# Performance work log

Measured on AMD Instinct MI355X. Metric: run time of the kernel, lower is better.

The kernel has to match this reference:

```python
import jax, jax.numpy as jnp
from jax import lax
import numpy as np

D, E, N, L = 192, 384, 16, 2
P_SZ, IMG, C_IN, K = 16, 224, 3, 3
NP = (IMG // P_SZ) ** 2          # 196 patches
M = NP + 1                        # +cls token
BATCH = 8


def setup_inputs() -> dict:
    key = jax.random.key(0)
    ks = iter(jax.random.split(key, 40))
    nrm = lambda shape, s=0.02: jax.random.normal(next(ks), shape, jnp.float32) * s
    inp = {
        "img": jax.random.normal(next(ks), (BATCH, C_IN, IMG, IMG), jnp.float32),
        "patch_w": nrm((C_IN * P_SZ * P_SZ, D)),
        "patch_b": jnp.zeros((D,), jnp.float32),
        "cls": jnp.zeros((1, 1, D), jnp.float32),
        "pos": nrm((1, M, D)),
        # per-layer stacked params (leading dim L)
        "ln_g": jnp.ones((L, D), jnp.float32), "ln_b": jnp.zeros((L, D), jnp.float32),
        "Wx": nrm((L, D, E)), "bx": jnp.zeros((L, E), jnp.float32),
        "Wz": nrm((L, D, E)), "bz": jnp.zeros((L, E), jnp.float32),
        "cwf": nrm((L, E, 1, K), 0.1), "cbf": jnp.zeros((L, E), jnp.float32),
        "cwb": nrm((L, E, 1, K), 0.1), "cbb": jnp.zeros((L, E), jnp.float32),
        "WBf": nrm((L, E, E * N)), "bBf": jnp.zeros((L, E * N), jnp.float32),
        "WCf": nrm((L, E, E * N)), "bCf": jnp.zeros((L, E * N), jnp.float32),
        "WDf": jnp.zeros((L, E, E), jnp.float32), "bDf": jnp.zeros((L, E), jnp.float32),
        "Af": nrm((L, E, N), 0.01), "dbf": jnp.zeros((L, E), jnp.float32),
        "WBb": nrm((L, E, E * N)), "bBb": jnp.zeros((L, E * N), jnp.float32),
        "WCb": nrm((L, E, E * N)), "bCb": jnp.zeros((L, E * N), jnp.float32),
        "WDb": jnp.zeros((L, E, E), jnp.float32), "bDb": jnp.zeros((L, E), jnp.float32),
        "Ab": nrm((L, E, N), 0.01), "dbb": jnp.zeros((L, E), jnp.float32),
        "Wout": nrm((L, E, D)), "bout": jnp.zeros((L, D), jnp.float32),
        "ng": jnp.ones((D,), jnp.float32), "nb": jnp.zeros((D,), jnp.float32),
    }
    return inp


def layernorm(x, g, b, eps=1e-5):
    mu = x.mean(-1, keepdims=True)
    var = ((x - mu) ** 2).mean(-1, keepdims=True)
    return (x - mu) * lax.rsqrt(var + eps) * g + b


def dwconv(x, w, b):
    # x: (B, M, E), w: (E, 1, K) depthwise, 'same' padding
    xc = jnp.transpose(x, (0, 2, 1))  # (B, E, M)
    pad = (w.shape[-1] - 1) // 2
    y = lax.conv_general_dilated(xc, w, (1,), [(pad, pad)],
                                 dimension_numbers=("NCH", "OIH", "NCH"),
                                 feature_group_count=w.shape[0])
    return jnp.transpose(y, (0, 2, 1)) + b


def ssm_recurrence(A, Bm, Cm, x):
    # A,Bm,Cm: (B,M,E,N); x: (B,M,E). Log-space prefix-product scan.
    eps = 1e-6
    signA = jnp.sign(A)
    absA = jnp.clip(jnp.abs(A), eps)
    logP = jnp.cumsum(jnp.log(absA), axis=1)
    P = jnp.cumprod(signA, axis=1) * jnp.exp(logP)
    invP = 1.0 / (P + eps)
    S = jnp.cumsum(invP * Bm * x[..., None], axis=1)
    h = P * S
    return (h * Cm).sum(-1)  # (B, M, E)


def vim_block(x, p, i):
    Bsz, Mseq, _ = x.shape
    xn = layernorm(x, p["ln_g"][i], p["ln_b"][i])
    xp = xn @ p["Wx"][i] + p["bx"][i]
    z = xn @ p["Wz"][i] + p["bz"][i]
    xf = jax.nn.silu(dwconv(xp, p["cwf"][i], p["cbf"][i]))
    xb = jax.nn.silu(dwconv(xp[:, ::-1], p["cwb"][i], p["cbb"][i])[:, ::-1])

    def branch(xs, WB, bB, WC, bC, WD, bD, Apar, db):
        Bm = (xs @ WB + bB).reshape(Bsz, Mseq, E, N)
        Cm = (xs @ WC + bC).reshape(Bsz, Mseq, E, N)
        Delta = jax.nn.softplus(xs @ WD + bD + db)          # (B,M,E)
        Afull = Delta[..., None] * Apar[None, None]          # (B,M,E,N)
        Bfull = Delta[..., None] * Bm
        return ssm_recurrence(Afull, Bfull, Cm, xs)

    y_f = branch(xf, p["WBf"][i], p["bBf"][i], p["WCf"][i], p["bCf"][i],
                 p["WDf"][i], p["bDf"][i], p["Af"][i], p["dbf"][i])
    y_b = branch(xb, p["WBb"][i], p["bBb"][i], p["WCb"][i], p["bCb"][i],
                 p["WDb"][i], p["bDb"][i], p["Ab"][i], p["dbb"][i])
    g = jax.nn.silu(z)
    y = (y_f + y_b) * g
    return y @ p["Wout"][i] + p["bout"][i] + x


def reference(img, patch_w, patch_b, cls, pos, ln_g, ln_b, Wx, bx, Wz, bz,
              cwf, cbf, cwb, cbb, WBf, bBf, WCf, bCf, WDf, bDf, Af, dbf,
              WBb, bBb, WCb, bCb, WDb, bDb, Ab, dbb, Wout, bout, ng, nb):
    Bsz = img.shape[0]
    hn = IMG // P_SZ
    # patchify (equivalent to Conv2d kernel=stride=patch): (B,3,H,W)->(B,NP,3*p*p)
    patches = img.reshape(Bsz, C_IN, hn, P_SZ, hn, P_SZ)
    patches = patches.transpose(0, 2, 4, 1, 3, 5).reshape(Bsz, NP, C_IN * P_SZ * P_SZ)
    x = patches @ patch_w + patch_b                           # (B,NP,D)
    x = jnp.concatenate([jnp.broadcast_to(cls, (Bsz, 1, D)), x], axis=1)
    x = x + pos
    p = dict(ln_g=ln_g, ln_b=ln_b, Wx=Wx, bx=bx, Wz=Wz, bz=bz, cwf=cwf, cbf=cbf,
             cwb=cwb, cbb=cbb, WBf=WBf, bBf=bBf, WCf=WCf, bCf=bCf, WDf=WDf,
             bDf=bDf, Af=Af, dbf=dbf, WBb=WBb, bBb=bBb, WCb=WCb, bCb=bCb,
             WDb=WDb, bDb=bDb, Ab=Ab, dbb=dbb, Wout=Wout, bout=bout)
    for i in range(L):
        x = vim_block(x, p, i)
    return layernorm(x, ng, nb)  # (B, M, D)
```

## Files before the change

### kernel.cpp

```cpp
#include <hip/hip_runtime.h>
#include <hip/hip_bf16.h>
#include <math.h>

#define BATCH   8
#define C_IN    3
#define IMG_SZ  224
#define P_SZ    16
#define NPATCH  196
#define MSEQ    197
#define DDIM    192
#define EDIM    384
#define NSTATE  16
#define ENDIM   (EDIM*NSTATE)
#define LLAYERS 2
#define ROWS    (BATCH*MSEQ)
#define PROWS   (BATCH*NPATCH)
#define PATCH_K (C_IN*P_SZ*P_SZ)
#define AP_ROWS 1664
#define MFRAGS  52
#define NFRAGS  192
#define KBLKS   24
#define FRAG    512

typedef unsigned short u16;
typedef __attribute__((ext_vector_type(8))) short bf16x8;
typedef __attribute__((ext_vector_type(16))) float f32x16;

__device__ __forceinline__ float silu_f(float x) { return x / (1.f + expf(-x)); }

__device__ __forceinline__ u16 f2bf(float f) {
    unsigned u = __float_as_uint(f);
    unsigned r = (u + 0x7FFFu + ((u >> 16) & 1u)) >> 16;
    return (u16)r;
}
__device__ __forceinline__ float bf2f(u16 h) {
    return __uint_as_float(((unsigned)h) << 16);
}

__global__ __launch_bounds__(256) void patchify_k(const float* __restrict__ img,
                                                  float* __restrict__ out) {
    int idx = blockIdx.x * 256 + threadIdx.x;
    if (idx >= PROWS * PATCH_K) return;
    int r = idx / PATCH_K, col = idx - r * PATCH_K;
    int b = r / NPATCH, p = r - b * NPATCH;
    int ph = p / 14, pw = p - ph * 14;
    int c = col >> 8, rem = col & 255, py = rem >> 4, px = rem & 15;
    out[idx] = img[((b * C_IN + c) * IMG_SZ + ph * P_SZ + py) * IMG_SZ + pw * P_SZ + px];
}

__global__ __launch_bounds__(256) void assemble_k(const float* __restrict__ xemb,
                                                  const float* __restrict__ cls,
                                                  const float* __restrict__ pos,
                                                  float* __restrict__ x) {
    int idx = blockIdx.x * 256 + threadIdx.x;
    if (idx >= ROWS * DDIM) return;
    int d = idx % DDIM;
    int bm = idx / DDIM;
    int m = bm % MSEQ, b = bm / MSEQ;
    float v;
    if (m == 0) v = cls[d];
    else        v = xemb[((b * NPATCH) + (m - 1)) * DDIM + d];
    x[idx] = v + pos[m * DDIM + d];
}

__global__ __launch_bounds__(256) void layernorm_k(const float* __restrict__ x,
                                                   const float* __restrict__ g,
                                                   const float* __restrict__ b,
                                                   float* __restrict__ o, int nrows) {
    int wave = threadIdx.x >> 6;
    int lane = threadIdx.x & 63;
    int row = blockIdx.x * 4 + wave;
    if (row >= nrows) return;
    const float* xr = x + (long)row * DDIM;
    float v0 = xr[lane], v1 = xr[lane + 64], v2 = xr[lane + 128];
    float s = v0 + v1 + v2;
    #pragma unroll
    for (int off = 1; off < 64; off <<= 1) s += __shfl_xor(s, off);
    float mu = s * (1.f / 192.f);
    float d0 = v0 - mu, d1 = v1 - mu, d2 = v2 - mu;
    float q = d0 * d0 + d1 * d1 + d2 * d2;
    #pragma unroll
    for (int off = 1; off < 64; off <<= 1) q += __shfl_xor(q, off);
    float inv = rsqrtf(q * (1.f / 192.f) + 1e-5f);
    float* orow = o + (long)row * DDIM;
    orow[lane]       = d0 * inv * g[lane]       + b[lane];
    orow[lane + 64]  = d1 * inv * g[lane + 64]  + b[lane + 64];
    orow[lane + 128] = d2 * inv * g[lane + 128] + b[lane + 128];
}

__global__ __launch_bounds__(256) void convA_k(const float* __restrict__ xf,
                                               const float* __restrict__ xb,
                                               u16* __restrict__ Af3,
                                               u16* __restrict__ Ab3) {
    int idx = blockIdx.x * 256 + threadIdx.x;
    if (idx >= MFRAGS * KBLKS * 64) return;
    int lane = idx & 63;
    int kb = (idx >> 6) % KBLKS;
    int mf = idx / (64 * KBLKS);
    int row = mf * 32 + (lane & 31);
    int k = kb * 16 + (lane >> 5) * 8;
    long fo = ((long)mf * KBLKS + kb) * FRAG + (long)lane * 8;
    const long plane = (long)MFRAGS * KBLKS * FRAG;
    #pragma unroll
    for (int s = 0; s < 2; ++s) {
        const float* src = s ? xb : xf;
        u16* out = s ? Ab3 : Af3;
        uint4 hq = {0,0,0,0}, mq = {0,0,0,0}, lq = {0,0,0,0};
        if (row < ROWS) {
            u16* hp = (u16*)&hq; u16* mp = (u16*)&mq; u16* lp = (u16*)&lq;
            const float* xr = src + (long)row * EDIM + k;
            #pragma unroll
            for (int j = 0; j < 8; ++j) {
                float x = xr[j];
                u16 hb = f2bf(x);        float fh = bf2f(hb);
                float r1 = x - fh;
                u16 mb = f2bf(r1);       float fm = bf2f(mb);
                u16 lb = f2bf(r1 - fm);
                hp[j] = hb; mp[j] = mb; lp[j] = lb;
            }
        }
        *(uint4*)&out[fo] = hq;
        *(uint4*)&out[plane + fo] = mq;
        *(uint4*)&out[2 * plane + fo] = lq;
    }
}

__global__ __launch_bounds__(256) void convWt_k(const float* __restrict__ W0,
                                                const float* __restrict__ W1,
                                                const float* __restrict__ W2,
                                                const float* __restrict__ W3,
                                                u16* __restrict__ Wt) {
    int z = blockIdx.z;
    const float* W = (z == 0) ? W0 : (z == 1) ? W1 : (z == 2) ? W2 : W3;
    const long plane = (long)NFRAGS * KBLKS * FRAG;
    u16* out = Wt + (long)z * 3L * plane;
    __shared__ float tile[64][65];
    int n0 = blockIdx.x * 64, k0 = blockIdx.y * 64;
    int t = threadIdx.x;
    #pragma unroll
    for (int i = 0; i < 16; ++i) {
        int id = t + 256 * i;
        int kk = id >> 6, nn = id & 63;
        tile[kk][nn] = W[(long)(k0 + kk) * ENDIM + n0 + nn];
    }
    __syncthreads();
    #pragma unroll
    for (int i = 0; i < 2; ++i) {
        int id = t + 256 * i;
        int nn = id >> 3, ch = id & 7;
        int n = n0 + nn;
        int kc = k0 + ch * 8;
        int nf = n >> 5, l31 = n & 31;
        int kb = kc >> 4, l5 = (kc >> 3) & 1;
        uint4 hq, mq, lq;
        u16* hp = (u16*)&hq; u16* mp = (u16*)&mq; u16* lp = (u16*)&lq;
        #pragma unroll
        for (int j = 0; j < 8; ++j) {
            float x = tile[ch * 8 + j][nn];
            u16 hb = f2bf(x);        float fh = bf2f(hb);
            float r1 = x - fh;
            u16 mb = f2bf(r1);       float fm = bf2f(mb);
            u16 lb = f2bf(r1 - fm);
            hp[j] = hb; mp[j] = mb; lp[j] = lb;
        }
        long fo = ((long)nf * KBLKS + kb) * FRAG + (long)(l5 * 32 + l31) * 8;
        *(uint4*)&out[fo] = hq;
        *(uint4*)&out[plane + fo] = mq;
        *(uint4*)&out[2 * plane + fo] = lq;
    }
}

__global__ __launch_bounds__(256) void gemm_mfma(
        const u16* __restrict__ A3,
        const u16* __restrict__ Wt0, const float* __restrict__ b0, float* __restrict__ C0,
        const u16* __restrict__ Wt1, const float* __restrict__ b1, float* __restrict__ C1) {
    const u16* Wt     = blockIdx.z ? Wt1 : Wt0;
    const float* bias = blockIdx.z ? b1 : b0;
    float* C          = blockIdx.z ? C1 : C0;
    int t = threadIdx.x;
    int lane = t & 63, wv = t >> 6;
    int wr = wv >> 1, wc = wv & 1;
    int l31 = lane & 31, l5 = lane >> 5;
    int mf0 = blockIdx.y * 4 + wr * 2;
    int nf0 = blockIdx.x * 4 + wc * 2;
    const u16* Ab = A3 + (long)lane * 8;
    const u16* Wb = Wt + (long)lane * 8;
    f32x16 acc[2][2] = {};

    for (int kb = 0; kb < KBLKS; ++kb) {
        bf16x8 af[2][3], wf[2][3];
        #pragma unroll
        for (int r = 0; r < 2; ++r)
            #pragma unroll
            for (int p = 0; p < 3; ++p)
                af[r][p] = *(const bf16x8*)(Ab + (((long)p * MFRAGS + mf0 + r) * KBLKS + kb) * FRAG);
        #pragma unroll
        for (int c = 0; c < 2; ++c)
            #pragma unroll
            for (int p = 0; p < 3; ++p)
                wf[c][p] = *(const bf16x8*)(Wb + (((long)p * NFRAGS + nf0 + c) * KBLKS + kb) * FRAG);
        #pragma unroll
        for (int r = 0; r < 2; ++r)
            #pragma unroll
            for (int c = 0; c < 2; ++c) {
                f32x16 d = acc[r][c];
                d = __builtin_amdgcn_mfma_f32_32x32x16_bf16(af[r][0], wf[c][0], d, 0, 0, 0);
                d = __builtin_amdgcn_mfma_f32_32x32x16_bf16(af[r][0], wf[c][1], d, 0, 0, 0);
                d = __builtin_amdgcn_mfma_f32_32x32x16_bf16(af[r][1], wf[c][0], d, 0, 0, 0);
                d = __builtin_amdgcn_mfma_f32_32x32x16_bf16(af[r][0], wf[c][2], d, 0, 0, 0);
                d = __builtin_amdgcn_mfma_f32_32x32x16_bf16(af[r][2], wf[c][0], d, 0, 0, 0);
                d = __builtin_amdgcn_mfma_f32_32x32x16_bf16(af[r][1], wf[c][1], d, 0, 0, 0);
                acc[r][c] = d;
            }
    }
    int rowBase = blockIdx.y * 128;
    long colBase = (long)blockIdx.x * 128;
    #pragma unroll
    for (int r = 0; r < 2; ++r) {
        int rb = rowBase + wr * 64 + r * 32 + 4 * l5;
        #pragma unroll
        for (int c = 0; c < 2; ++c) {
            long cb = colBase + wc * 64 + c * 32 + l31;
            float bv = bias[cb];
            #pragma unroll
            for (int i = 0; i < 16; ++i) {
                int rr = rb + (i & 3) + 8 * (i >> 2);
                if (rr < ROWS) C[(long)rr * ENDIM + cb] = acc[r][c][i] + bv;
            }
        }
    }
}

#define SBK 16
template<bool SP, bool HASB2, bool HASRES>
__global__ __launch_bounds__(64) void gemm_s(const float* __restrict__ A0,
                                             const float* __restrict__ W0,
                                             const float* __restrict__ b10,
                                             const float* __restrict__ b20,
                                             const float* __restrict__ r0,
                                             float* __restrict__ C0,
                                             const float* __restrict__ A1,
                                             const float* __restrict__ W1,
                                             const float* __restrict__ b11,
                                             const float* __restrict__ b21,
                                             const float* __restrict__ r1,
                                             float* __restrict__ C1,
                                             int M, int N, int K) {
    const float* A  = blockIdx.z ? A1  : A0;
    const float* W  = blockIdx.z ? W1  : W0;
    const float* bp = blockIdx.z ? b11 : b10;
    const float* b2 = blockIdx.z ? b21 : b20;
    const float* rp = blockIdx.z ? r1  : r0;
    float*       C  = blockIdx.z ? C1  : C0;
    __shared__ float As[2][SBK][36];
    __shared__ float Wsh[2][SBK][36];
    int t = threadIdx.x;
    int tx = t & 7, ty = t >> 3;
    int rowBase = blockIdx.y * 32;
    long colBase = (long)blockIdx.x * 32;
    int rA = t >> 2, kqA = (t & 3) << 2;
    int kW = t >> 3, nqW = (t & 7) << 2;
    float acc[4][4] = {};
    int r0i = rowBase + rA, r1i = r0i + 16;

    auto loadA = [&](int k0, float4& a0, float4& a1) {
        a0 = make_float4(0.f,0.f,0.f,0.f); a1 = a0;
        if (r0i < M) a0 = *(const float4*)&A[(long)r0i * K + k0 + kqA];
        if (r1i < M) a1 = *(const float4*)&A[(long)r1i * K + k0 + kqA];
    };
    auto stage = [&](int buf, float4 a0, float4 a1, float4 w0, float4 w1) {
        As[buf][kqA + 0][rA] = a0.x; As[buf][kqA + 1][rA] = a0.y;
        As[buf][kqA + 2][rA] = a0.z; As[buf][kqA + 3][rA] = a0.w;
        As[buf][kqA + 0][rA + 16] = a1.x; As[buf][kqA + 1][rA + 16] = a1.y;
        As[buf][kqA + 2][rA + 16] = a1.z; As[buf][kqA + 3][rA + 16] = a1.w;
        *(float4*)&Wsh[buf][kW][nqW]     = w0;
        *(float4*)&Wsh[buf][kW + 8][nqW] = w1;
    };
    auto compute = [&](int buf) {
        #pragma unroll
        for (int kk = 0; kk < SBK; ++kk) {
            float4 av = *(const float4*)&As[buf][kk][ty << 2];
            float4 wv = *(const float4*)&Wsh[buf][kk][tx << 2];
            float ar[4] = {av.x, av.y, av.z, av.w};
            float wr[4] = {wv.x, wv.y, wv.z, wv.w};
            #pragma unroll
            for (int i = 0; i < 4; ++i)
                #pragma unroll
                for (int j = 0; j < 4; ++j) acc[i][j] += ar[i] * wr[j];
        }
    };

    {
        float4 a0, a1;
        loadA(0, a0, a1);
        float4 w0 = *(const float4*)&W[(long)kW * N + colBase + nqW];
        float4 w1 = *(const float4*)&W[(long)(kW + 8) * N + colBase + nqW];
        stage(0, a0, a1, w0, w1);
    }
    __syncthreads();
    int cur = 0;
    int nt = K / SBK;
    for (int kt = 1; kt < nt; ++kt) {
        int k0 = kt * SBK;
        float4 a0, a1;
        loadA(k0, a0, a1);
        float4 w0 = *(const float4*)&W[(long)(k0 + kW) * N + colBase + nqW];
        float4 w1 = *(const float4*)&W[(long)(k0 + kW + 8) * N + colBase + nqW];
        compute(cur);
        stage(cur ^ 1, a0, a1, w0, w1);
        __syncthreads();
        cur ^= 1;
    }
    compute(cur);

    #pragma unroll
    for (int i = 0; i < 4; ++i) {
        int r = rowBase + (ty << 2) + i;
        if (r >= M) break;
        long cb = colBase + (tx << 2);
        float vv[4];
        #pragma unroll
        for (int j = 0; j < 4; ++j) {
            float v = acc[i][j] + bp[cb + j];
            if (HASB2) v += b2[cb + j];
            if (SP) {
                double vd = (double)v;
                v = (float)(log1p(exp(-fabs(vd))) + fmax(vd, 0.0));
            }
            if (HASRES) v += rp[(long)r * N + cb + j];
            vv[j] = v;
        }
        float4 o; o.x = vv[0]; o.y = vv[1]; o.z = vv[2]; o.w = vv[3];
        *(float4*)&C[(long)r * N + cb] = o;
    }
}

__global__ __launch_bounds__(256) void dwconv_k(const float* __restrict__ xp,
                                                const float* __restrict__ wf,
                                                const float* __restrict__ bf,
                                                const float* __restrict__ wb,
                                                const float* __restrict__ bb,
                                                float* __restrict__ xf,
                                                float* __restrict__ xb) {
    int idx = blockIdx.x * 256 + threadIdx.x;
    if (idx >= ROWS * EDIM) return;
    int e = idx % EDIM;
    int bm = idx / EDIM;
    int m = bm % MSEQ, b = bm / MSEQ;
    const float* base = xp + (long)b * MSEQ * EDIM + e;
    float xm1 = (m > 0)        ? base[(m - 1) * EDIM] : 0.f;
    float x0  =                  base[m * EDIM];
    float xp1 = (m < MSEQ - 1) ? base[(m + 1) * EDIM] : 0.f;
    float f = wf[e * 3 + 0] * xm1 + wf[e * 3 + 1] * x0 + wf[e * 3 + 2] * xp1 + bf[e];
    float r = wb[e * 3 + 0] * xp1 + wb[e * 3 + 1] * x0 + wb[e * 3 + 2] * xm1 + bb[e];
    xf[idx] = silu_f(f);
    xb[idx] = silu_f(r);
}

__global__ __launch_bounds__(256) void ssm_scan_k(const float* __restrict__ Bm,
                                                  const float* __restrict__ Cm,
                                                  const float* __restrict__ Dlt,
                                                  const float* __restrict__ xs,
                                                  const float* __restrict__ Apar,
                                                  float* __restrict__ y,
                                                  const float* __restrict__ yother,
                                                  const float* __restrict__ zg,
                                                  float* __restrict__ ycomb) {
#pragma clang fp contract(off)
    __shared__ float lgP[MSEQ][17];
    __shared__ float trm[MSEQ][17];
    __shared__ signed char sgn[MSEQ][17];
    int be = blockIdx.x;
    int b = be / EDIM, e = be - b * EDIM;
    int t = threadIdx.x;
    int n0 = t & 15;
    float Ap = Apar[e * NSTATE + n0];
    const long dxBase = (long)b * MSEQ * EDIM + e;
    const long bcBase = (long)b * MSEQ * ENDIM + e * NSTATE;

    for (int idx = t; idx < MSEQ * NSTATE; idx += 256) {
        int m = idx >> 4;
        float delta = Dlt[dxBase + (long)m * EDIM];
        float A = delta * Ap;
        float sa = (A > 0.f) ? 1.f : ((A < 0.f) ? -1.f : 0.f);
        float absA = fmaxf(fabsf(A), 1e-6f);
        lgP[m][n0] = (float)log((double)absA);
        sgn[m][n0] = (signed char)sa;
    }
    __syncthreads();
    if (t < NSTATE) {
        float cl = 0.f, cs = 1.f;
        for (int m = 0; m < MSEQ; ++m) {
            float sa = (float)sgn[m][t];
            cs = cs * sa;
            cl = cl + lgP[m][t];
            lgP[m][t] = cl;
            sgn[m][t] = (signed char)cs;
        }
    }
    __syncthreads();
    for (int idx = t; idx < MSEQ * NSTATE; idx += 256) {
        int m = idx >> 4;
        float cl = lgP[m][n0];
        float cs = (float)sgn[m][n0];
        float ex = (float)exp((double)cl);
        float P = cs * ex;
        float tt = P + 1e-6f;
        float invP = 1.0f / tt;
        float delta = Dlt[dxBase + (long)m * EDIM];
        float xv = xs[dxBase + (long)m * EDIM];
        float Bv = Bm[bcBase + (long)m * ENDIM + n0];
        float Bfull = delta * Bv;
        float t1 = invP * Bfull;
        float t2 = t1 * xv;
        trm[m][n0] = t2;
        lgP[m][n0] = P;
    }
    __syncthreads();
    if (t < NSTATE) {
        float S = 0.f;
        for (int m = 0; m < MSEQ; ++m) {
            S = S + trm[m][t];
            float h = lgP[m][t] * S;
            trm[m][t] = h;
        }
    }
    __syncthreads();
    for (int m = t; m < MSEQ; m += 256) {
        const float* cp = &Cm[bcBase + (long)m * ENDIM];
        float a[16];
        #pragma unroll
        for (int n = 0; n < 16; ++n) a[n] = trm[m][n] * cp[n];
        float b0 = a[0] + a[8],  b1 = a[1] + a[9];
        float b2v = a[2] + a[10], b3 = a[3] + a[11];
        float b4 = a[4] + a[12], b5 = a[5] + a[13];
        float b6 = a[6] + a[14], b7 = a[7] + a[15];
        float c0 = b0 + b1, c2 = b2v + b3, c4 = b4 + b5, c6 = b6 + b7;
        float d0 = c0 + c2, d4 = c4 + c6;
        float val = d0 + d4;
        long o = dxBase + (long)m * EDIM;
        if (ycomb) ycomb[o] = (yother[o] + val) * silu_f(zg[o]);
        else       y[o] = val;
    }
}

extern "C" void kernel_launch(void* const* d_in, const int* in_sizes, int n_in,
                              void* d_out, int out_size, void* d_ws, size_t ws_size,
                              hipStream_t stream) {
    const float* img     = (const float*)d_in[0];
    const float* patch_w = (const float*)d_in[1];
    const float* patch_b = (const float*)d_in[2];
    const float* cls     = (const float*)d_in[3];
    const float* pos     = (const float*)d_in[4];
    const float* ln_g    = (const float*)d_in[5];
    const float* ln_b    = (const float*)d_in[6];
    const float* Wx  = (const float*)d_in[7];  const float* bx  = (const float*)d_in[8];
    const float* Wz  = (const float*)d_in[9];  const float* bz  = (const float*)d_in[10];
    const float* cwf = (const float*)d_in[11]; const float* cbf = (const float*)d_in[12];
    const float* cwb = (const float*)d_in[13]; const float* cbb = (const float*)d_in[14];
    const float* WBf = (const float*)d_in[15]; const float* bBf = (const float*)d_in[16];
    const float* WCf = (const float*)d_in[17]; const float* bCf = (const float*)d_in[18];
    const float* WDf = (const float*)d_in[19]; const float* bDf = (const float*)d_in[20];
    const float* Af  = (const float*)d_in[21]; const float* dbf = (const float*)d_in[22];
    const float* WBb = (const float*)d_in[23]; const float* bBb = (const float*)d_in[24];
    const float* WCb = (const float*)d_in[25]; const float* bCb = (const float*)d_in[26];
    const float* WDb = (const float*)d_in[27]; const float* bDb = (const float*)d_in[28];
    const float* Ab  = (const float*)d_in[29]; const float* dbb = (const float*)d_in[30];
    const float* Wout= (const float*)d_in[31]; const float* bout= (const float*)d_in[32];
    const float* ng  = (const float*)d_in[33]; const float* nb  = (const float*)d_in[34];

    float* ws = (float*)d_ws;
    float* xA   = ws;
    float* xB   = xA  + (size_t)ROWS * DDIM;
    float* xn   = xB  + (size_t)ROWS * DDIM;
    float* xp   = xn  + (size_t)ROWS * DDIM;
    float* zb   = xp  + (size_t)ROWS * EDIM;
    float* xfb  = zb  + (size_t)ROWS * EDIM;
    float* xbb  = xfb + (size_t)ROWS * EDIM;
    float* yfb  = xbb + (size_t)ROWS * EDIM;
    float* ybb  = yfb + (size_t)ROWS * EDIM;
    float* ycb  = ybb + (size_t)ROWS * EDIM;
    float* dlt  = ycb + (size_t)ROWS * EDIM;
    float* dlt2 = dlt + (size_t)ROWS * EDIM;
    float* Bmb  = dlt2 + (size_t)ROWS * EDIM;
    float* Cmb  = Bmb + (size_t)ROWS * ENDIM;
    u16*   Af3  = (u16*)(Cmb + (size_t)ROWS * ENDIM);
    u16*   Ab3  = Af3 + 3L * MFRAGS * KBLKS * FRAG;
    u16*   Wt4  = Ab3 + 3L * MFRAGS * KBLKS * FRAG;
    float* patches = Bmb;
    float* xemb    = Bmb + (size_t)PROWS * PATCH_K;

    const long WtSz = 3L * NFRAGS * KBLKS * FRAG;

    patchify_k<<<(PROWS * PATCH_K + 255) / 256, 256, 0, stream>>>(img, patches);
    {
        dim3 g(DDIM / 32, (PROWS + 31) / 32, 1);
        gemm_s<false, false, false><<<g, 64, 0, stream>>>(
            patches, patch_w, patch_b, nullptr, nullptr, xemb,
            patches, patch_w, patch_b, nullptr, nullptr, xemb,
            PROWS, DDIM, PATCH_K);
    }
    assemble_k<<<(ROWS * DDIM + 255) / 256, 256, 0, stream>>>(xemb, cls, pos, xA);

    float* cur = xA; float* nxt = xB;
    for (int i = 0; i < LLAYERS; ++i) {
        layernorm_k<<<(ROWS + 3) / 4, 256, 0, stream>>>(cur, ln_g + i * DDIM, ln_b + i * DDIM, xn, ROWS);
        {
            dim3 g(EDIM / 32, (ROWS + 31) / 32, 2);
            gemm_s<false, false, false><<<g, 64, 0, stream>>>(
                xn, Wx + (size_t)i * DDIM * EDIM, bx + i * EDIM, nullptr, nullptr, xp,
                xn, Wz + (size_t)i * DDIM * EDIM, bz + i * EDIM, nullptr, nullptr, zb,
                ROWS, EDIM, DDIM);
        }
        dwconv_k<<<(ROWS * EDIM + 255) / 256, 256, 0, stream>>>(xp, cwf + i * EDIM * 3, cbf + i * EDIM,
                                                                cwb + i * EDIM * 3, cbb + i * EDIM, xfb, xbb);
        convA_k<<<(MFRAGS * KBLKS * 64 + 255) / 256, 256, 0, stream>>>(xfb, xbb, Af3, Ab3);
        {
            dim3 g(EDIM / 32, (ROWS + 31) / 32, 2);
            gemm_s<true, true, false><<<g, 64, 0, stream>>>(
                xfb, WDf + (size_t)i * EDIM * EDIM, bDf + i * EDIM, dbf + i * EDIM, nullptr, dlt,
                xbb, WDb + (size_t)i * EDIM * EDIM, bDb + i * EDIM, dbb + i * EDIM, nullptr, dlt2,
                ROWS, EDIM, EDIM);
        }
        {
            dim3 g(ENDIM / 64, EDIM / 64, 4);
            convWt_k<<<g, 256, 0, stream>>>(
                WBf + (size_t)i * EDIM * ENDIM, WCf + (size_t)i * EDIM * ENDIM,
                WBb + (size_t)i * EDIM * ENDIM, WCb + (size_t)i * EDIM * ENDIM, Wt4);
        }
        {
            dim3 g(ENDIM / 128, AP_ROWS / 128, 2);
            gemm_mfma<<<g, 256, 0, stream>>>(
                Af3,
                Wt4 + 0 * WtSz, bBf + i * ENDIM, Bmb,
                Wt4 + 1 * WtSz, bCf + i * ENDIM, Cmb);
        }
        ssm_scan_k<<<BATCH * EDIM, 256, 0, stream>>>(Bmb, Cmb, dlt, xfb, Af + i * EDIM * NSTATE,
                                                     yfb, nullptr, nullptr, nullptr);
        {
            dim3 g(ENDIM / 128, AP_ROWS / 128, 2);
            gemm_mfma<<<g, 256, 0, stream>>>(
                Ab3,
                Wt4 + 2 * WtSz, bBb + i * ENDIM, Bmb,
                Wt4 + 3 * WtSz, bCb + i * ENDIM, Cmb);
        }
        ssm_scan_k<<<BATCH * EDIM, 256, 0, stream>>>(Bmb, Cmb, dlt2, xbb, Ab + i * EDIM * NSTATE,
                                                     ybb, yfb, zb, ycb);
        {
            dim3 g(DDIM / 32, (ROWS + 31) / 32, 1);
            gemm_s<false, false, true><<<g, 64, 0, stream>>>(
                ycb, Wout + (size_t)i * EDIM * DDIM, bout + i * DDIM, nullptr, cur, nxt,
                ycb, Wout + (size_t)i * EDIM * DDIM, bout + i * DDIM, nullptr, cur, nxt,
                ROWS, DDIM, EDIM);
        }
        float* t = cur; cur = nxt; nxt = t;
    }
    layernorm_k<<<(ROWS + 3) / 4, 256, 0, stream>>>(cur, ng, nb, (float*)d_out, ROWS);
}
```

Measured before the change: 933.0 us.

## Stage GEMM fragments through shared memory with register prefetch

The MFMA GEMM now has each wave load a distinct slice of the block's A and W fragments for the current k-block into LDS, then every wave reads its fragments from LDS. Before, each wave fetched its fragments from global memory directly, so wave pairs loaded the same data twice. The next k-block is prefetched into registers while the current one is computed, which cuts redundant global and L2 traffic and overlaps loads with MFMA work. The cost is two barriers per k-block and 24KB of LDS per block.

```diff
diff --git a/kernel.cpp b/kernel.cpp
--- a/kernel.cpp
+++ b/kernel.cpp
@@ -177,28 +177,66 @@
     const u16* Wt     = blockIdx.z ? Wt1 : Wt0;
     const float* bias = blockIdx.z ? b1 : b0;
     float* C          = blockIdx.z ? C1 : C0;
+    __shared__ u16 lsb[24 * FRAG];
     int t = threadIdx.x;
     int lane = t & 63, wv = t >> 6;
     int wr = wv >> 1, wc = wv & 1;
     int l31 = lane & 31, l5 = lane >> 5;
-    int mf0 = blockIdx.y * 4 + wr * 2;
-    int nf0 = blockIdx.x * 4 + wc * 2;
-    const u16* Ab = A3 + (long)lane * 8;
-    const u16* Wb = Wt + (long)lane * 8;
+    int mf0 = blockIdx.y * 4;
+    int nf0 = blockIdx.x * 4;
     f32x16 acc[2][2] = {};
 
+    long srcBase[6];
+    {
+        #pragma unroll
+        for (int i = 0; i < 6; ++i) {
+            int f = wv * 6 + i;
+            if (f < 12)
+                srcBase[i] = (((long)(f >> 2) * MFRAGS + mf0 + (f & 3)) * KBLKS) * FRAG + (long)lane * 8;
+            else {
+                int g = f - 12;
+                srcBase[i] = (((long)(g >> 2) * NFRAGS + nf0 + (g & 3)) * KBLKS) * FRAG + (long)lane * 8;
+            }
+        }
+    }
+    const u16* gsrc = (wv < 2) ? A3 : Wt;
+    u16* ldst = &lsb[(wv * 6) * FRAG + lane * 8];
+
+    uint4 r0, r1, r2, r3, r4, r5;
+    auto gload = [&](int kb) {
+        long o = (long)kb * FRAG;
+        r0 = *(const uint4*)(gsrc + srcBase[0] + o);
+        r1 = *(const uint4*)(gsrc + srcBase[1] + o);
+        r2 = *(const uint4*)(gsrc + srcBase[2] + o);
+        r3 = *(const uint4*)(gsrc + srcBase[3] + o);
+        r4 = *(const uint4*)(gsrc + srcBase[4] + o);
+        r5 = *(const uint4*)(gsrc + srcBase[5] + o);
+    };
+    auto swrite = [&]() {
+        *(uint4*)(ldst + 0 * FRAG) = r0;
+        *(uint4*)(ldst + 1 * FRAG) = r1;
+        *(uint4*)(ldst + 2 * FRAG) = r2;
+        *(uint4*)(ldst + 3 * FRAG) = r3;
+        *(uint4*)(ldst + 4 * FRAG) = r4;
+        *(uint4*)(ldst + 5 * FRAG) = r5;
+    };
+
+    gload(0);
     for (int kb = 0; kb < KBLKS; ++kb) {
+        swrite();
+        __syncthreads();
+        if (kb + 1 < KBLKS) gload(kb + 1);
         bf16x8 af[2][3], wf[2][3];
         #pragma unroll
         for (int r = 0; r < 2; ++r)
             #pragma unroll
             for (int p = 0; p < 3; ++p)
-                af[r][p] = *(const bf16x8*)(Ab + (((long)p * MFRAGS + mf0 + r) * KBLKS + kb) * FRAG);
+                af[r][p] = *(const bf16x8*)&lsb[(p * 4 + wr * 2 + r) * FRAG + lane * 8];
         #pragma unroll
         for (int c = 0; c < 2; ++c)
             #pragma unroll
             for (int p = 0; p < 3; ++p)
-                wf[c][p] = *(const bf16x8*)(Wb + (((long)p * NFRAGS + nf0 + c) * KBLKS + kb) * FRAG);
+                wf[c][p] = *(const bf16x8*)&lsb[(12 + p * 4 + wc * 2 + c) * FRAG + lane * 8];
         #pragma unroll
         for (int r = 0; r < 2; ++r)
             #pragma unroll
@@ -212,6 +250,7 @@
                 d = __builtin_amdgcn_mfma_f32_32x32x16_bf16(af[r][1], wf[c][1], d, 0, 0, 0);
                 acc[r][c] = d;
             }
+        __syncthreads();
     }
     int rowBase = blockIdx.y * 128;
     long colBase = (long)blockIdx.x * 128;
```

New measurement: 924.4 us, median of 3. About the same (-0.9%).
